# Kernel tuning notes

Hardware: AMD Instinct MI355X
Metric: run time of the kernel (lower is better)

## Reference

```python
import jax, jax.numpy as jnp
import numpy as np

STEPLIM = 20   # module steplim; loop runs while iter <= steplim -> steplim+1 iterations
TOL = 1e-4     # early-stopping tolerance on change in mean NN error


def _nn1(pc1, pc2):
    """1-NN of each point in pc1 [B,N,3] within pc2 [B,M,3] under L2 norm.
    Uses the GEMM form ||a||^2 + ||b||^2 - 2 a.b instead of materializing the
    [B,N,M,3] broadcasted difference tensor. Returns (min_dist [B,N], idx [B,N])."""
    d2 = (jnp.sum(pc1 * pc1, axis=-1)[..., :, None]
          + jnp.sum(pc2 * pc2, axis=-1)[..., None, :]
          - 2.0 * jnp.einsum('bnd,bmd->bnm', pc1, pc2))
    d2 = jnp.maximum(d2, 1e-12)                  # clamp FP cancellation negatives
    idx = jnp.argmin(d2, axis=-1)                # [B, N]
    dmin = jnp.sqrt(jnp.take_along_axis(d2, idx[..., None], axis=-1)[..., 0])
    return dmin, idx


def _kabsch(src, dst):
    """Rigid transform (R, t) minimizing ||R@src + t - dst|| via SVD (EPnP._points_transform)."""
    c1 = jnp.mean(src, axis=-2, keepdims=True)   # [B,1,3]
    c2 = jnp.mean(dst, axis=-2, keepdims=True)
    H = jnp.einsum('bni,bnj->bij', src - c1, dst - c2)          # [B,3,3]
    U, S, Vt = jnp.linalg.svd(H, full_matrices=False)
    det = jnp.linalg.det(jnp.einsum('bki,bjk->bij', Vt, U))     # det(V U^T)
    d = jnp.sign(det)
    D = jnp.stack([jnp.ones_like(d), jnp.ones_like(d), d], axis=-1)  # reflection fix
    R = jnp.einsum('bki,bk,bjk->bij', Vt, D, U)                 # V diag(1,1,d) U^T
    t = c2[..., 0, :] - jnp.einsum('bij,bj->bi', R, c1[..., 0, :])
    return R, t


def _icp(p1, p2):
    B = p1.shape[0]

    def step(carry, _):
        pc, err, done = carry
        dmin, idx = _nn1(pc, p2)
        # errnew = sum(sum(values)/len(values)): mean over batch of per-point sums
        errnew = jnp.sum(dmin) / B
        # source quirk: uses the LAST batch element's indices for all batches
        matched = p2[:, idx[-1], :]                              # [B,N,3]
        R, t = _kabsch(pc, matched)
        pc_new = jnp.einsum('bij,bnj->bni', R, pc) + t[:, None, :]
        # torch loop updates temppc BEFORE the break check, then freezes
        pc_out = jnp.where(done, pc, pc_new)
        err_out = jnp.where(done, err, errnew)
        done_out = done | (jnp.abs(err - errnew) < TOL)
        return (pc_out, err_out, done_out), None

    init = (p1, jnp.asarray(0.0, p1.dtype), jnp.asarray(False))
    (pc, _, _), _ = jax.lax.scan(step, init, None, length=STEPLIM + 1)
    R, t = _kabsch(p1, pc)
    return jnp.concatenate([R, t[..., None]], axis=-1)           # [B,3,4] = [R | t]


def setup_inputs() -> dict:
    key = jax.random.key(0)
    k1, k2 = jax.random.split(key)
    p1 = jax.random.normal(k1, (1, 8192, 3), dtype=jnp.float32)
    p2 = jax.random.normal(k2, (1, 8192, 3), dtype=jnp.float32)
    return {"p1": p1, "p2": p2}


def reference(p1, p2):
    return _icp(p1, p2)
```

## Files before the change

kernel.cpp:

```cpp
#include <hip/hip_runtime.h>
#include <math.h>

#define N_PTS 8192
#define ICP_STEPS 21
#define ICP_TOL 1e-4

#define NBLK 256
#define BSIZE 1024
#define QPW 8

struct IcpCtl {
  double err;
  double Rc[9];
  double tc[3];
  int done;
};

__global__ __launch_bounds__(256) void icp_prep(const float* __restrict__ p2,
                                                float4* __restrict__ p2aug,
                                                IcpCtl* __restrict__ ctl) {
  int t = blockIdx.x * 256 + threadIdx.x;
  float x = p2[3*t], y = p2[3*t+1], z = p2[3*t+2];
  p2aug[t] = make_float4(x, y, z, fmaf(x, x, fmaf(y, y, z*z)));
  if (t == 0) {
    ctl->err = 0.0; ctl->done = 0;
    #pragma unroll
    for (int i = 0; i < 9; ++i) ctl->Rc[i] = (i % 4 == 0) ? 1.0 : 0.0;
    ctl->tc[0] = ctl->tc[1] = ctl->tc[2] = 0.0;
  }
}

__device__ __forceinline__ void kabsch_solve(const double* s, double* R, double* T) {
  const double n = (double)N_PTS;
  const double c1x = s[1]/n, c1y = s[2]/n, c1z = s[3]/n;
  const double c2x = s[4]/n, c2y = s[5]/n, c2z = s[6]/n;
  const double h00 = s[7]  - n*c1x*c2x, h01 = s[8]  - n*c1x*c2y, h02 = s[9]  - n*c1x*c2z;
  const double h10 = s[10] - n*c1y*c2x, h11 = s[11] - n*c1y*c2y, h12 = s[12] - n*c1y*c2z;
  const double h20 = s[13] - n*c1z*c2x, h21 = s[14] - n*c1z*c2y, h22 = s[15] - n*c1z*c2z;

  double a00 = h00*h00 + h10*h10 + h20*h20;
  double a01 = h00*h01 + h10*h11 + h20*h21;
  double a02 = h00*h02 + h10*h12 + h20*h22;
  double a11 = h01*h01 + h11*h11 + h21*h21;
  double a12 = h01*h02 + h11*h12 + h21*h22;
  double a22 = h02*h02 + h12*h12 + h22*h22;

  double v00=1.0, v01=0.0, v02=0.0;
  double v10=0.0, v11=1.0, v12=0.0;
  double v20=0.0, v21=0.0, v22=1.0;

#define ROT3(app, aqq, apq, arp, arq, vpa, vqa, vpb, vqb, vpc, vqc)              \
  {                                                                              \
    double apq_ = apq;                                                           \
    if (fabs(apq_) > 1e-300) {                                                   \
      double tau = (aqq - app) / (2.0 * apq_);                                   \
      double tt  = (tau >= 0.0 ? 1.0 : -1.0) / (fabs(tau) + sqrt(1.0 + tau*tau));\
      double c_  = 1.0 / sqrt(1.0 + tt*tt), sn = tt * c_;                        \
      app -= tt * apq_;  aqq += tt * apq_;  apq = 0.0;                           \
      double t1 = arp, t2 = arq;                                                 \
      arp = c_*t1 - sn*t2;  arq = sn*t1 + c_*t2;                                 \
      t1 = vpa; t2 = vqa; vpa = c_*t1 - sn*t2; vqa = sn*t1 + c_*t2;              \
      t1 = vpb; t2 = vqb; vpb = c_*t1 - sn*t2; vqb = sn*t1 + c_*t2;              \
      t1 = vpc; t2 = vqc; vpc = c_*t1 - sn*t2; vqc = sn*t1 + c_*t2;              \
    }                                                                            \
  }

  #pragma unroll
  for (int sweep = 0; sweep < 6; ++sweep) {
    ROT3(a00, a11, a01, a02, a12, v00, v01, v10, v11, v20, v21);
    ROT3(a00, a22, a02, a01, a12, v00, v02, v10, v12, v20, v22);
    ROT3(a11, a22, a12, a01, a02, v01, v02, v11, v12, v21, v22);
  }
#undef ROT3

  double l0 = a00, l1 = a11, l2 = a22;
  double e0x=v00, e0y=v10, e0z=v20;
  double e1x=v01, e1y=v11, e1z=v21;
  double e2x=v02, e2y=v12, e2z=v22;
#define CSWAP(la, lb, xa, ya, za, xb, yb, zb)                                    \
  if (lb > la) { double t_;                                                      \
    t_ = la; la = lb; lb = t_;  t_ = xa; xa = xb; xb = t_;                       \
    t_ = ya; ya = yb; yb = t_;  t_ = za; za = zb; zb = t_; }
  CSWAP(l0, l1, e0x, e0y, e0z, e1x, e1y, e1z);
  CSWAP(l0, l2, e0x, e0y, e0z, e2x, e2y, e2z);
  CSWAP(l1, l2, e1x, e1y, e1z, e2x, e2y, e2z);
#undef CSWAP

  double detV = e0x*(e1y*e2z - e1z*e2y) - e0y*(e1x*e2z - e1z*e2x)
              + e0z*(e1x*e2y - e1y*e2x);
  const double dsg = (detV >= 0.0) ? 1.0 : -1.0;

  double u0x = h00*e0x + h01*e0y + h02*e0z;
  double u0y = h10*e0x + h11*e0y + h12*e0z;
  double u0z = h20*e0x + h21*e0y + h22*e0z;
  double n0 = sqrt(u0x*u0x + u0y*u0y + u0z*u0z);
  if (!(n0 > 1e-150)) {
    R[0]=1.0; R[1]=0.0; R[2]=0.0; R[3]=0.0; R[4]=1.0; R[5]=0.0;
    R[6]=0.0; R[7]=0.0; R[8]=1.0;
    T[0]=c2x-c1x; T[1]=c2y-c1y; T[2]=c2z-c1z;
    return;
  }
  u0x /= n0; u0y /= n0; u0z /= n0;
  double u1x = h00*e1x + h01*e1y + h02*e1z;
  double u1y = h10*e1x + h11*e1y + h12*e1z;
  double u1z = h20*e1x + h21*e1y + h22*e1z;
  const double d10 = u1x*u0x + u1y*u0y + u1z*u0z;
  u1x -= d10*u0x; u1y -= d10*u0y; u1z -= d10*u0z;
  double n1 = sqrt(u1x*u1x + u1y*u1y + u1z*u1z);
  if (!(n1 > 1e-150)) {
    R[0]=1.0; R[1]=0.0; R[2]=0.0; R[3]=0.0; R[4]=1.0; R[5]=0.0;
    R[6]=0.0; R[7]=0.0; R[8]=1.0;
    T[0]=c2x-c1x; T[1]=c2y-c1y; T[2]=c2z-c1z;
    return;
  }
  u1x /= n1; u1y /= n1; u1z /= n1;
  const double u2x = u0y*u1z - u0z*u1y;
  const double u2y = u0z*u1x - u0x*u1z;
  const double u2z = u0x*u1y - u0y*u1x;

  R[0] = e0x*u0x + e1x*u1x + dsg*e2x*u2x;
  R[1] = e0x*u0y + e1x*u1y + dsg*e2x*u2y;
  R[2] = e0x*u0z + e1x*u1z + dsg*e2x*u2z;
  R[3] = e0y*u0x + e1y*u1x + dsg*e2y*u2x;
  R[4] = e0y*u0y + e1y*u1y + dsg*e2y*u2y;
  R[5] = e0y*u0z + e1y*u1z + dsg*e2y*u2z;
  R[6] = e0z*u0x + e1z*u1x + dsg*e2z*u2x;
  R[7] = e0z*u0y + e1z*u1y + dsg*e2z*u2y;
  R[8] = e0z*u0z + e1z*u1z + dsg*e2z*u2z;
  T[0] = c2x - (R[0]*c1x + R[1]*c1y + R[2]*c1z);
  T[1] = c2y - (R[3]*c1x + R[4]*c1y + R[5]*c1z);
  T[2] = c2z - (R[6]*c1x + R[7]*c1y + R[8]*c1z);
}

__global__ __launch_bounds__(BSIZE, 4) void icp_iter(const float* __restrict__ p1,
                                                     const float4* __restrict__ p2aug,
                                                     const IcpCtl* __restrict__ ctl,
                                                     double* __restrict__ part) {
  if (ctl->done) return;
  __shared__ float4 cand[N_PTS];
  __shared__ unsigned long long pkbuf[32][4];
  __shared__ float4 qlds[32];
  __shared__ double pairbuf[32][17];

  const int tid  = threadIdx.x;
  const int lane = tid & 63;
  const int w    = tid >> 6;
  const int g    = w >> 2;
  const int s    = w & 3;

  #pragma unroll
  for (int k = 0; k < 8; ++k) {
    const int i = (k << 10) + tid;
    cand[i] = p2aug[i];
  }

  const double R0 = ctl->Rc[0], R1 = ctl->Rc[1], R2 = ctl->Rc[2];
  const double R3 = ctl->Rc[3], R4 = ctl->Rc[4], R5 = ctl->Rc[5];
  const double R6 = ctl->Rc[6], R7 = ctl->Rc[7], R8 = ctl->Rc[8];
  const double T0 = ctl->tc[0], T1 = ctl->tc[1], T2 = ctl->tc[2];

  const int qbase = (blockIdx.x << 5) + (g << 3);
  float axv[QPW], ayv[QPW], azv[QPW], best[QPW];
  int bidx[QPW];
  float qxr[QPW], qyr[QPW], qzr[QPW];
  #pragma unroll
  for (int j = 0; j < QPW; ++j) {
    const int q = qbase + j;
    const double X = (double)p1[3*q], Y = (double)p1[3*q+1], Z = (double)p1[3*q+2];
    qxr[j] = (float)(R0*X + R1*Y + R2*Z + T0);
    qyr[j] = (float)(R3*X + R4*Y + R5*Z + T1);
    qzr[j] = (float)(R6*X + R7*Y + R8*Z + T2);
    axv[j] = -2.f*qxr[j]; ayv[j] = -2.f*qyr[j]; azv[j] = -2.f*qzr[j];
    best[j] = __builtin_inff(); bidx[j] = 0;
  }
  if (s == 0 && lane == 0) {
    #pragma unroll
    for (int j = 0; j < QPW; ++j)
      qlds[(g << 3) + j] = make_float4(qxr[j], qyr[j], qzr[j], 0.f);
  }
  __syncthreads();

  const int cb = s << 11;
  #pragma unroll 8
  for (int k = 0; k < 32; ++k) {
    const int cidx = cb + (k << 6) + lane;
    float4 c = cand[cidx];
    #pragma unroll
    for (int j = 0; j < QPW; ++j) {
      float d = fmaf(axv[j], c.x, fmaf(ayv[j], c.y, fmaf(azv[j], c.z, c.w)));
      if (d < best[j]) { best[j] = d; bidx[j] = cidx; }
    }
  }

  unsigned long long pk[QPW];
  #pragma unroll
  for (int j = 0; j < QPW; ++j) {
    unsigned u = __float_as_uint(best[j]);
    u ^= (unsigned)((int)u >> 31) | 0x80000000u;
    pk[j] = ((unsigned long long)u << 32) | (unsigned)bidx[j];
  }
  #pragma unroll
  for (int j = 0; j < QPW; ++j) {
    #pragma unroll
    for (int o = 1; o < 64; o <<= 1) {
      unsigned long long other = __shfl_xor(pk[j], o, 64);
      pk[j] = (other < pk[j]) ? other : pk[j];
    }
  }
  if (lane == 0) {
    #pragma unroll
    for (int j = 0; j < QPW; ++j)
      pkbuf[(g << 3) + j][s] = pk[j];
  }
  __syncthreads();

  if (tid < 32) {
    unsigned long long m = pkbuf[tid][0];
    unsigned long long m1 = pkbuf[tid][1]; m = (m1 < m) ? m1 : m;
    unsigned long long m2 = pkbuf[tid][2]; m = (m2 < m) ? m2 : m;
    unsigned long long m3 = pkbuf[tid][3]; m = (m3 < m) ? m3 : m;
    const unsigned idx = (unsigned)(m & 0xffffffffull);
    const float4 q4 = qlds[tid];
    const float4 b4 = cand[idx];
    const double ax = q4.x, ay = q4.y, az = q4.z;
    const double bx = b4.x, by = b4.y, bz = b4.z;
    const double d2 = (ax*ax + ay*ay + az*az) + (bx*bx + by*by + bz*bz)
                    - 2.0*(ax*bx + ay*by + az*bz);
    pairbuf[tid][0]  = sqrt(fmax(d2, 1e-12));
    pairbuf[tid][1]  = ax;    pairbuf[tid][2]  = ay;    pairbuf[tid][3]  = az;
    pairbuf[tid][4]  = bx;    pairbuf[tid][5]  = by;    pairbuf[tid][6]  = bz;
    pairbuf[tid][7]  = ax*bx; pairbuf[tid][8]  = ax*by; pairbuf[tid][9]  = ax*bz;
    pairbuf[tid][10] = ay*bx; pairbuf[tid][11] = ay*by; pairbuf[tid][12] = ay*bz;
    pairbuf[tid][13] = az*bx; pairbuf[tid][14] = az*by; pairbuf[tid][15] = az*bz;
  }
  __syncthreads();

  if (tid < 16) {
    double ssum = 0.0;
    #pragma unroll
    for (int i = 0; i < 32; ++i) ssum += pairbuf[i][tid];
    part[(blockIdx.x << 4) + tid] = ssum;
  }
}

__device__ __forceinline__ void block_reduce16(double* v, double* tot, double* lds) {
  const int lane = threadIdx.x & 63;
  const int w    = threadIdx.x >> 6;
  #pragma unroll
  for (int q = 0; q < 16; ++q) {
    double x = v[q];
    for (int o = 32; o > 0; o >>= 1) x += __shfl_down(x, o, 64);
    if (lane == 0) lds[w*16 + q] = x;
  }
  __syncthreads();
  if (threadIdx.x < 16)
    tot[threadIdx.x] = lds[threadIdx.x] + lds[16 + threadIdx.x]
                     + lds[32 + threadIdx.x] + lds[48 + threadIdx.x];
  __syncthreads();
}

__global__ __launch_bounds__(256) void icp_solve(IcpCtl* __restrict__ ctl,
                                                 const double* __restrict__ part,
                                                 float* __restrict__ out) {
  if (ctl->done) return;
  __shared__ double lds[64];
  __shared__ double tot[16];
  double v[16];
  const double* row = part + (threadIdx.x << 4);
  #pragma unroll
  for (int c = 0; c < 16; ++c) v[c] = row[c];
  block_reduce16(v, tot, lds);

  if (threadIdx.x == 0) {
    double s[16];
    #pragma unroll
    for (int i = 0; i < 16; ++i) s[i] = tot[i];
    double R[9], T[3];
    kabsch_solve(s, R, T);
    double Rc[9], tc[3], Rn[9], tn[3];
    #pragma unroll
    for (int i = 0; i < 9; ++i) Rc[i] = ctl->Rc[i];
    #pragma unroll
    for (int i = 0; i < 3; ++i) tc[i] = ctl->tc[i];
    #pragma unroll
    for (int i = 0; i < 3; ++i) {
      #pragma unroll
      for (int j = 0; j < 3; ++j)
        Rn[3*i+j] = R[3*i+0]*Rc[0+j] + R[3*i+1]*Rc[3+j] + R[3*i+2]*Rc[6+j];
      tn[i] = R[3*i+0]*tc[0] + R[3*i+1]*tc[1] + R[3*i+2]*tc[2] + T[i];
    }
    #pragma unroll
    for (int i = 0; i < 9; ++i) ctl->Rc[i] = Rn[i];
    #pragma unroll
    for (int i = 0; i < 3; ++i) ctl->tc[i] = tn[i];
    const double errnew = s[0];
    ctl->done = (fabs(ctl->err - errnew) < ICP_TOL) ? 1 : 0;
    ctl->err  = errnew;
    #pragma unroll
    for (int i = 0; i < 3; ++i) {
      out[4*i + 0] = (float)Rn[3*i + 0];
      out[4*i + 1] = (float)Rn[3*i + 1];
      out[4*i + 2] = (float)Rn[3*i + 2];
      out[4*i + 3] = (float)tn[i];
    }
  }
}

extern "C" void kernel_launch(void* const* d_in, const int* in_sizes, int n_in,
                              void* d_out, int out_size, void* d_ws, size_t ws_size,
                              hipStream_t stream) {
  const float* p1 = (const float*)d_in[0];
  const float* p2 = (const float*)d_in[1];
  float* out = (float*)d_out;

  char* ws = (char*)d_ws;
  float4* p2aug = (float4*)ws;
  IcpCtl* ctl   = (IcpCtl*)(ws + 128*1024);
  double* part  = (double*)(ws + 128*1024 + 512);

  icp_prep<<<N_PTS/256, 256, 0, stream>>>(p2, p2aug, ctl);
  for (int it = 0; it < ICP_STEPS; ++it) {
    icp_iter<<<NBLK, BSIZE, 0, stream>>>(p1, p2aug, ctl, part);
    icp_solve<<<1, 256, 0, stream>>>(ctl, part, out);
  }
}
```

Baseline: 552.2 us.

## Fuse per-iteration Kabsch solve into NN kernel via last-block atomic ticket

Drops the separate single-block solve kernel. Each block now atomically adds its 16 partial sums into a global accumulator, and a ticket counter picks the last block to finish, which runs the Kabsch solve, updates the pose and resets the accumulator. This halves the number of kernel launches per ICP step and removes the launch gap and serial reduction kernel between steps. In exchange it adds contention on 16 double atomics and relies on memory-ordering correctness. Summation order is now nondeterministic across runs.

```diff
diff --git a/kernel.cpp b/kernel.cpp
--- a/kernel.cpp
+++ b/kernel.cpp
@@ -8,22 +8,26 @@
 #define NBLK 256
 #define BSIZE 1024
 #define QPW 8
+#define ACC_STRIDE 8
 
 struct IcpCtl {
   double err;
   double Rc[9];
   double tc[3];
   int done;
+  unsigned ticket;
 };
 
 __global__ __launch_bounds__(256) void icp_prep(const float* __restrict__ p2,
                                                 float4* __restrict__ p2aug,
-                                                IcpCtl* __restrict__ ctl) {
+                                                IcpCtl* __restrict__ ctl,
+                                                double* __restrict__ acc) {
   int t = blockIdx.x * 256 + threadIdx.x;
   float x = p2[3*t], y = p2[3*t+1], z = p2[3*t+2];
   p2aug[t] = make_float4(x, y, z, fmaf(x, x, fmaf(y, y, z*z)));
+  if (t < 16 * ACC_STRIDE) acc[t] = 0.0;
   if (t == 0) {
-    ctl->err = 0.0; ctl->done = 0;
+    ctl->err = 0.0; ctl->done = 0; ctl->ticket = 0u;
     #pragma unroll
     for (int i = 0; i < 9; ++i) ctl->Rc[i] = (i % 4 == 0) ? 1.0 : 0.0;
     ctl->tc[0] = ctl->tc[1] = ctl->tc[2] = 0.0;
@@ -134,13 +138,16 @@
 
 __global__ __launch_bounds__(BSIZE, 4) void icp_iter(const float* __restrict__ p1,
                                                      const float4* __restrict__ p2aug,
-                                                     const IcpCtl* __restrict__ ctl,
-                                                     double* __restrict__ part) {
+                                                     IcpCtl* __restrict__ ctl,
+                                                     double* __restrict__ acc,
+                                                     float* __restrict__ out) {
   if (ctl->done) return;
   __shared__ float4 cand[N_PTS];
   __shared__ unsigned long long pkbuf[32][4];
   __shared__ float4 qlds[32];
   __shared__ double pairbuf[32][17];
+  __shared__ double tot[16];
+  __shared__ int lastFlag;
 
   const int tid  = threadIdx.x;
   const int lane = tid & 63;
@@ -239,49 +246,28 @@
     double ssum = 0.0;
     #pragma unroll
     for (int i = 0; i < 32; ++i) ssum += pairbuf[i][tid];
-    part[(blockIdx.x << 4) + tid] = ssum;
-  }
-}
-
-__device__ __forceinline__ void block_reduce16(double* v, double* tot, double* lds) {
-  const int lane = threadIdx.x & 63;
-  const int w    = threadIdx.x >> 6;
-  #pragma unroll
-  for (int q = 0; q < 16; ++q) {
-    double x = v[q];
-    for (int o = 32; o > 0; o >>= 1) x += __shfl_down(x, o, 64);
-    if (lane == 0) lds[w*16 + q] = x;
-  }
-  __syncthreads();
-  if (threadIdx.x < 16)
-    tot[threadIdx.x] = lds[threadIdx.x] + lds[16 + threadIdx.x]
-                     + lds[32 + threadIdx.x] + lds[48 + threadIdx.x];
-  __syncthreads();
-}
-
-__global__ __launch_bounds__(256) void icp_solve(IcpCtl* __restrict__ ctl,
-                                                 const double* __restrict__ part,
-                                                 float* __restrict__ out) {
-  if (ctl->done) return;
-  __shared__ double lds[64];
-  __shared__ double tot[16];
-  double v[16];
-  const double* row = part + (threadIdx.x << 4);
-  #pragma unroll
-  for (int c = 0; c < 16; ++c) v[c] = row[c];
-  block_reduce16(v, tot, lds);
-
-  if (threadIdx.x == 0) {
-    double s[16];
-    #pragma unroll
-    for (int i = 0; i < 16; ++i) s[i] = tot[i];
+    atomicAdd(acc + tid * ACC_STRIDE, ssum);
+  }
+  if (tid == 0) {
+    asm volatile("s_waitcnt vmcnt(0)" ::: "memory");
+    unsigned old = __hip_atomic_fetch_add(&ctl->ticket, 1u,
+                      __ATOMIC_RELAXED, __HIP_MEMORY_SCOPE_AGENT);
+    lastFlag = (old == NBLK - 1u) ? 1 : 0;
+  }
+  __syncthreads();
+  if (!lastFlag) return;
+
+  if (tid < 16) tot[tid] = atomicAdd(acc + tid * ACC_STRIDE, 0.0);
+  __syncthreads();
+  if (tid == 0) {
+    double sm[16];
+    #pragma unroll
+    for (int i = 0; i < 16; ++i) sm[i] = tot[i];
     double R[9], T[3];
-    kabsch_solve(s, R, T);
-    double Rc[9], tc[3], Rn[9], tn[3];
-    #pragma unroll
-    for (int i = 0; i < 9; ++i) Rc[i] = ctl->Rc[i];
-    #pragma unroll
-    for (int i = 0; i < 3; ++i) tc[i] = ctl->tc[i];
+    kabsch_solve(sm, R, T);
+    double Rc[9] = {R0,R1,R2,R3,R4,R5,R6,R7,R8};
+    double tc[3] = {T0,T1,T2};
+    double Rn[9], tn[3];
     #pragma unroll
     for (int i = 0; i < 3; ++i) {
       #pragma unroll
@@ -293,7 +279,7 @@
     for (int i = 0; i < 9; ++i) ctl->Rc[i] = Rn[i];
     #pragma unroll
     for (int i = 0; i < 3; ++i) ctl->tc[i] = tn[i];
-    const double errnew = s[0];
+    const double errnew = sm[0];
     ctl->done = (fabs(ctl->err - errnew) < ICP_TOL) ? 1 : 0;
     ctl->err  = errnew;
     #pragma unroll
@@ -303,6 +289,9 @@
       out[4*i + 2] = (float)Rn[3*i + 2];
       out[4*i + 3] = (float)tn[i];
     }
+    #pragma unroll
+    for (int i = 0; i < 16; ++i) acc[i * ACC_STRIDE] = 0.0;
+    ctl->ticket = 0u;
   }
 }
 
@@ -316,11 +305,9 @@
   char* ws = (char*)d_ws;
   float4* p2aug = (float4*)ws;
   IcpCtl* ctl   = (IcpCtl*)(ws + 128*1024);
-  double* part  = (double*)(ws + 128*1024 + 512);
-
-  icp_prep<<<N_PTS/256, 256, 0, stream>>>(p2, p2aug, ctl);
-  for (int it = 0; it < ICP_STEPS; ++it) {
-    icp_iter<<<NBLK, BSIZE, 0, stream>>>(p1, p2aug, ctl, part);
-    icp_solve<<<1, 256, 0, stream>>>(ctl, part, out);
-  }
+  double* acc   = (double*)(ws + 128*1024 + 512);
+
+  icp_prep<<<N_PTS/256, 256, 0, stream>>>(p2, p2aug, ctl, acc);
+  for (int it = 0; it < ICP_STEPS; ++it)
+    icp_iter<<<NBLK, BSIZE, 0, stream>>>(p1, p2aug, ctl, acc, out);
 }
```

Measured after the change: 585.4 us. 1.06x slower.

## Fuse per-iteration Kabsch solve into the next NN-search kernel with ping-pong state

Applied to the files above, without the earlier changes.

Removes the separate single-block solve launch after each ICP iteration. Every block of the next iteration kernel now reduces the previous iteration's partial sums, solves the Kabsch transform and composes it redundantly, then proceeds with its nearest-neighbour search. State and partial buffers are double-buffered so reads and writes don't race, and a final small kernel produces the output. This trades about 20 launch and serialization gaps for redundant per-block reduction work and extra L2 reads of the partials. The occupancy hint in launch_bounds is also dropped.

```diff
diff --git a/kernel.cpp b/kernel.cpp
--- a/kernel.cpp
+++ b/kernel.cpp
@@ -9,24 +9,24 @@
 #define BSIZE 1024
 #define QPW 8
 
-struct IcpCtl {
-  double err;
+struct IcpSt {
   double Rc[9];
   double tc[3];
+  double err;
   int done;
 };
 
 __global__ __launch_bounds__(256) void icp_prep(const float* __restrict__ p2,
                                                 float4* __restrict__ p2aug,
-                                                IcpCtl* __restrict__ ctl) {
+                                                IcpSt* __restrict__ st0) {
   int t = blockIdx.x * 256 + threadIdx.x;
   float x = p2[3*t], y = p2[3*t+1], z = p2[3*t+2];
   p2aug[t] = make_float4(x, y, z, fmaf(x, x, fmaf(y, y, z*z)));
   if (t == 0) {
-    ctl->err = 0.0; ctl->done = 0;
-    #pragma unroll
-    for (int i = 0; i < 9; ++i) ctl->Rc[i] = (i % 4 == 0) ? 1.0 : 0.0;
-    ctl->tc[0] = ctl->tc[1] = ctl->tc[2] = 0.0;
+    #pragma unroll
+    for (int i = 0; i < 9; ++i) st0->Rc[i] = (i % 4 == 0) ? 1.0 : 0.0;
+    st0->tc[0] = st0->tc[1] = st0->tc[2] = 0.0;
+    st0->err = 0.0; st0->done = 0;
   }
 }
 
@@ -132,12 +132,38 @@
   T[2] = c2z - (R[6]*c1x + R[7]*c1y + R[8]*c1z);
 }
 
-__global__ __launch_bounds__(BSIZE, 4) void icp_iter(const float* __restrict__ p1,
-                                                     const float4* __restrict__ p2aug,
-                                                     const IcpCtl* __restrict__ ctl,
-                                                     double* __restrict__ part) {
-  if (ctl->done) return;
+__device__ __forceinline__ void solve_compose(const double* s, const IcpSt* stIn,
+                                              double* Rn, double* tn,
+                                              double* errnew, int* dn) {
+  double R[9], T[3];
+  kabsch_solve(s, R, T);
+  double Rc[9], tc[3];
+  #pragma unroll
+  for (int i = 0; i < 9; ++i) Rc[i] = stIn->Rc[i];
+  #pragma unroll
+  for (int i = 0; i < 3; ++i) tc[i] = stIn->tc[i];
+  #pragma unroll
+  for (int i = 0; i < 3; ++i) {
+    #pragma unroll
+    for (int j = 0; j < 3; ++j)
+      Rn[3*i+j] = R[3*i+0]*Rc[0+j] + R[3*i+1]*Rc[3+j] + R[3*i+2]*Rc[6+j];
+    tn[i] = R[3*i+0]*tc[0] + R[3*i+1]*tc[1] + R[3*i+2]*tc[2] + T[i];
+  }
+  *errnew = s[0];
+  *dn = (fabs(stIn->err - *errnew) < ICP_TOL) ? 1 : 0;
+}
+
+__global__ __launch_bounds__(BSIZE) void icp_iter(const float* __restrict__ p1,
+                                                  const float4* __restrict__ p2aug,
+                                                  const IcpSt* __restrict__ stIn,
+                                                  IcpSt* __restrict__ stOut,
+                                                  const double* __restrict__ partIn,
+                                                  double* __restrict__ partOut,
+                                                  const int k) {
   __shared__ float4 cand[N_PTS];
+  __shared__ double redbuf[64];
+  __shared__ double RT[12];
+  __shared__ int sdone;
   __shared__ unsigned long long pkbuf[32][4];
   __shared__ float4 qlds[32];
   __shared__ double pairbuf[32][17];
@@ -148,16 +174,72 @@
   const int g    = w >> 2;
   const int s    = w & 3;
 
-  #pragma unroll
-  for (int k = 0; k < 8; ++k) {
-    const int i = (k << 10) + tid;
+  if (stIn->done) {
+    if (blockIdx.x == 0 && tid == 0) {
+      #pragma unroll
+      for (int i = 0; i < 9; ++i) stOut->Rc[i] = stIn->Rc[i];
+      #pragma unroll
+      for (int i = 0; i < 3; ++i) stOut->tc[i] = stIn->tc[i];
+      stOut->err = stIn->err; stOut->done = 1;
+    }
+    return;
+  }
+
+  #pragma unroll
+  for (int k2 = 0; k2 < 8; ++k2) {
+    const int i = (k2 << 10) + tid;
     cand[i] = p2aug[i];
   }
 
-  const double R0 = ctl->Rc[0], R1 = ctl->Rc[1], R2 = ctl->Rc[2];
-  const double R3 = ctl->Rc[3], R4 = ctl->Rc[4], R5 = ctl->Rc[5];
-  const double R6 = ctl->Rc[6], R7 = ctl->Rc[7], R8 = ctl->Rc[8];
-  const double T0 = ctl->tc[0], T1 = ctl->tc[1], T2 = ctl->tc[2];
+  double R0, R1, R2, R3, R4, R5, R6, R7, R8, T0, T1, T2;
+  if (k > 0) {
+    double vv[16];
+    if (tid < 256) {
+      const double* row = partIn + (tid << 4);
+      #pragma unroll
+      for (int c = 0; c < 16; ++c) vv[c] = row[c];
+    } else {
+      #pragma unroll
+      for (int c = 0; c < 16; ++c) vv[c] = 0.0;
+    }
+    if (w < 4) {
+      #pragma unroll
+      for (int q = 0; q < 16; ++q) {
+        double x = vv[q];
+        for (int o = 32; o > 0; o >>= 1) x += __shfl_down(x, o, 64);
+        if (lane == 0) redbuf[w*16 + q] = x;
+      }
+    }
+    __syncthreads();
+    if (tid == 0) {
+      double sm[16];
+      #pragma unroll
+      for (int i = 0; i < 16; ++i)
+        sm[i] = redbuf[i] + redbuf[16+i] + redbuf[32+i] + redbuf[48+i];
+      double Rn[9], tn[3], errnew; int dn;
+      solve_compose(sm, stIn, Rn, tn, &errnew, &dn);
+      #pragma unroll
+      for (int i = 0; i < 9; ++i) stOut->Rc[i] = Rn[i];
+      #pragma unroll
+      for (int i = 0; i < 3; ++i) stOut->tc[i] = tn[i];
+      stOut->err = errnew; stOut->done = dn;
+      #pragma unroll
+      for (int i = 0; i < 9; ++i) RT[i] = Rn[i];
+      RT[9] = tn[0]; RT[10] = tn[1]; RT[11] = tn[2];
+      sdone = dn;
+    }
+    __syncthreads();
+    if (sdone) return;
+    R0 = RT[0]; R1 = RT[1]; R2 = RT[2];
+    R3 = RT[3]; R4 = RT[4]; R5 = RT[5];
+    R6 = RT[6]; R7 = RT[7]; R8 = RT[8];
+    T0 = RT[9]; T1 = RT[10]; T2 = RT[11];
+  } else {
+    R0 = stIn->Rc[0]; R1 = stIn->Rc[1]; R2 = stIn->Rc[2];
+    R3 = stIn->Rc[3]; R4 = stIn->Rc[4]; R5 = stIn->Rc[5];
+    R6 = stIn->Rc[6]; R7 = stIn->Rc[7]; R8 = stIn->Rc[8];
+    T0 = stIn->tc[0]; T1 = stIn->tc[1]; T2 = stIn->tc[2];
+  }
 
   const int qbase = (blockIdx.x << 5) + (g << 3);
   float axv[QPW], ayv[QPW], azv[QPW], best[QPW];
@@ -182,8 +264,8 @@
 
   const int cb = s << 11;
   #pragma unroll 8
-  for (int k = 0; k < 32; ++k) {
-    const int cidx = cb + (k << 6) + lane;
+  for (int kk = 0; kk < 32; ++kk) {
+    const int cidx = cb + (kk << 6) + lane;
     float4 c = cand[cidx];
     #pragma unroll
     for (int j = 0; j < QPW; ++j) {
@@ -239,13 +321,35 @@
     double ssum = 0.0;
     #pragma unroll
     for (int i = 0; i < 32; ++i) ssum += pairbuf[i][tid];
-    part[(blockIdx.x << 4) + tid] = ssum;
-  }
-}
-
-__device__ __forceinline__ void block_reduce16(double* v, double* tot, double* lds) {
+    partOut[(blockIdx.x << 4) + tid] = ssum;
+  }
+}
+
+__global__ __launch_bounds__(256) void icp_final(const IcpSt* __restrict__ stIn,
+                                                 const double* __restrict__ partIn,
+                                                 float* __restrict__ out) {
+  __shared__ double lds[64];
+  __shared__ double tot[16];
   const int lane = threadIdx.x & 63;
   const int w    = threadIdx.x >> 6;
+
+  if (stIn->done) {
+    if (threadIdx.x == 0) {
+      #pragma unroll
+      for (int i = 0; i < 3; ++i) {
+        out[4*i + 0] = (float)stIn->Rc[3*i + 0];
+        out[4*i + 1] = (float)stIn->Rc[3*i + 1];
+        out[4*i + 2] = (float)stIn->Rc[3*i + 2];
+        out[4*i + 3] = (float)stIn->tc[i];
+      }
+    }
+    return;
+  }
+
+  double v[16];
+  const double* row = partIn + (threadIdx.x << 4);
+  #pragma unroll
+  for (int c = 0; c < 16; ++c) v[c] = row[c];
   #pragma unroll
   for (int q = 0; q < 16; ++q) {
     double x = v[q];
@@ -257,45 +361,13 @@
     tot[threadIdx.x] = lds[threadIdx.x] + lds[16 + threadIdx.x]
                      + lds[32 + threadIdx.x] + lds[48 + threadIdx.x];
   __syncthreads();
-}
-
-__global__ __launch_bounds__(256) void icp_solve(IcpCtl* __restrict__ ctl,
-                                                 const double* __restrict__ part,
-                                                 float* __restrict__ out) {
-  if (ctl->done) return;
-  __shared__ double lds[64];
-  __shared__ double tot[16];
-  double v[16];
-  const double* row = part + (threadIdx.x << 4);
-  #pragma unroll
-  for (int c = 0; c < 16; ++c) v[c] = row[c];
-  block_reduce16(v, tot, lds);
 
   if (threadIdx.x == 0) {
-    double s[16];
-    #pragma unroll
-    for (int i = 0; i < 16; ++i) s[i] = tot[i];
-    double R[9], T[3];
-    kabsch_solve(s, R, T);
-    double Rc[9], tc[3], Rn[9], tn[3];
-    #pragma unroll
-    for (int i = 0; i < 9; ++i) Rc[i] = ctl->Rc[i];
-    #pragma unroll
-    for (int i = 0; i < 3; ++i) tc[i] = ctl->tc[i];
-    #pragma unroll
-    for (int i = 0; i < 3; ++i) {
-      #pragma unroll
-      for (int j = 0; j < 3; ++j)
-        Rn[3*i+j] = R[3*i+0]*Rc[0+j] + R[3*i+1]*Rc[3+j] + R[3*i+2]*Rc[6+j];
-      tn[i] = R[3*i+0]*tc[0] + R[3*i+1]*tc[1] + R[3*i+2]*tc[2] + T[i];
-    }
-    #pragma unroll
-    for (int i = 0; i < 9; ++i) ctl->Rc[i] = Rn[i];
-    #pragma unroll
-    for (int i = 0; i < 3; ++i) ctl->tc[i] = tn[i];
-    const double errnew = s[0];
-    ctl->done = (fabs(ctl->err - errnew) < ICP_TOL) ? 1 : 0;
-    ctl->err  = errnew;
+    double sm[16];
+    #pragma unroll
+    for (int i = 0; i < 16; ++i) sm[i] = tot[i];
+    double Rn[9], tn[3], errnew; int dn;
+    solve_compose(sm, stIn, Rn, tn, &errnew, &dn);
     #pragma unroll
     for (int i = 0; i < 3; ++i) {
       out[4*i + 0] = (float)Rn[3*i + 0];
@@ -315,12 +387,22 @@
 
   char* ws = (char*)d_ws;
   float4* p2aug = (float4*)ws;
-  IcpCtl* ctl   = (IcpCtl*)(ws + 128*1024);
-  double* part  = (double*)(ws + 128*1024 + 512);
-
-  icp_prep<<<N_PTS/256, 256, 0, stream>>>(p2, p2aug, ctl);
-  for (int it = 0; it < ICP_STEPS; ++it) {
-    icp_iter<<<NBLK, BSIZE, 0, stream>>>(p1, p2aug, ctl, part);
-    icp_solve<<<1, 256, 0, stream>>>(ctl, part, out);
-  }
-}
+  IcpSt* st0    = (IcpSt*)(ws + 128*1024);
+  IcpSt* st1    = (IcpSt*)(ws + 128*1024 + 256);
+  double* part0 = (double*)(ws + 128*1024 + 1024);
+  double* part1 = (double*)(ws + 128*1024 + 1024 + 32*1024);
+
+  IcpSt* st[2]    = { st0, st1 };
+  double* part[2] = { part0, part1 };
+
+  icp_prep<<<N_PTS/256, 256, 0, stream>>>(p2, p2aug, st0);
+  for (int k = 0; k < ICP_STEPS; ++k) {
+    const IcpSt* stIn   = (k == 0) ? st0 : st[(k-1) & 1];
+    IcpSt* stOut        = st[k & 1];
+    const double* pIn   = part[(k+1) & 1];
+    double* pOut        = part[k & 1];
+    if (k == 0) stOut = st1;
+    icp_iter<<<NBLK, BSIZE, 0, stream>>>(p1, p2aug, stIn, stOut, pIn, pOut, k);
+  }
+  icp_final<<<1, 256, 0, stream>>>(st[0], part[0], out);
+}
```

Result: no change. 546.7 us (-1.0%).

## Replace full-LDS NN kernel with chunked, register-prefetched 256-thread blocks

Applied to the files above, without the earlier changes.

The nearest-neighbour kernel changes from 256 blocks of 1024 threads, each staging all 8192 candidates in LDS, to 512 blocks of 256 threads. Each block handles 16 queries, four per wave, and streams candidates through a 2048-entry LDS chunk, prefetching the next chunk into registers while the current one is scanned. The aim is to cut the per-block LDS footprint and the cost of the big up-front load, giving more resident blocks and overlapping global loads with compute. In exchange each wave now scans all candidates for only 4 queries, so candidate reuse per LDS read drops. The solve kernel is widened to 512 threads to reduce the doubled number of partials.

```diff
diff --git a/kernel.cpp b/kernel.cpp
--- a/kernel.cpp
+++ b/kernel.cpp
@@ -5,9 +5,11 @@
 #define ICP_STEPS 21
 #define ICP_TOL 1e-4
 
-#define NBLK 256
-#define BSIZE 1024
-#define QPW 8
+#define NNB 512
+#define QPB 16
+#define QPWv 4
+#define CH 2048
+#define NCH 4
 
 struct IcpCtl {
   double err;
@@ -27,6 +29,113 @@
     #pragma unroll
     for (int i = 0; i < 9; ++i) ctl->Rc[i] = (i % 4 == 0) ? 1.0 : 0.0;
     ctl->tc[0] = ctl->tc[1] = ctl->tc[2] = 0.0;
+  }
+}
+
+__global__ __launch_bounds__(256) void icp_nn(const float* __restrict__ p1,
+                                              const float4* __restrict__ p2aug,
+                                              const IcpCtl* __restrict__ ctl,
+                                              double* __restrict__ part) {
+  if (ctl->done) return;
+  __shared__ float4 cand[CH];
+  __shared__ unsigned long long pkbuf[4][5];
+  __shared__ float4 qlds[QPB];
+  __shared__ double pairbuf[QPB][17];
+
+  const int tid  = threadIdx.x;
+  const int lane = tid & 63;
+  const int w    = tid >> 6;
+
+  const double R0 = ctl->Rc[0], R1 = ctl->Rc[1], R2 = ctl->Rc[2];
+  const double R3 = ctl->Rc[3], R4 = ctl->Rc[4], R5 = ctl->Rc[5];
+  const double R6 = ctl->Rc[6], R7 = ctl->Rc[7], R8 = ctl->Rc[8];
+  const double T0 = ctl->tc[0], T1 = ctl->tc[1], T2 = ctl->tc[2];
+
+  const int qb = blockIdx.x * QPB + (w << 2);
+  float axv[QPWv], ayv[QPWv], azv[QPWv], best[QPWv];
+  int bidx[QPWv];
+  #pragma unroll
+  for (int j = 0; j < QPWv; ++j) {
+    const int q = qb + j;
+    const double X = (double)p1[3*q], Y = (double)p1[3*q+1], Z = (double)p1[3*q+2];
+    const float qx = (float)(R0*X + R1*Y + R2*Z + T0);
+    const float qy = (float)(R3*X + R4*Y + R5*Z + T1);
+    const float qz = (float)(R6*X + R7*Y + R8*Z + T2);
+    axv[j] = -2.f*qx; ayv[j] = -2.f*qy; azv[j] = -2.f*qz;
+    best[j] = __builtin_inff(); bidx[j] = 0;
+    if (lane == 0) qlds[(w << 2) + j] = make_float4(qx, qy, qz, 0.f);
+  }
+
+  float4 pf[8];
+  #pragma unroll
+  for (int k = 0; k < 8; ++k) pf[k] = p2aug[(k << 8) + tid];
+  for (int cb = 0; cb < NCH; ++cb) {
+    #pragma unroll
+    for (int k = 0; k < 8; ++k) cand[(k << 8) + tid] = pf[k];
+    __syncthreads();
+    if (cb + 1 < NCH) {
+      #pragma unroll
+      for (int k = 0; k < 8; ++k)
+        pf[k] = p2aug[((cb + 1) << 11) + (k << 8) + tid];
+    }
+    const int cbase = cb << 11;
+    #pragma unroll 8
+    for (int kk = 0; kk < 32; ++kk) {
+      const int cidx = cbase + (kk << 6) + lane;
+      float4 c = cand[(kk << 6) + lane];
+      #pragma unroll
+      for (int j = 0; j < QPWv; ++j) {
+        float d = fmaf(axv[j], c.x, fmaf(ayv[j], c.y, fmaf(azv[j], c.z, c.w)));
+        if (d < best[j]) { best[j] = d; bidx[j] = cidx; }
+      }
+    }
+    __syncthreads();
+  }
+
+  unsigned long long pk[QPWv];
+  #pragma unroll
+  for (int j = 0; j < QPWv; ++j) {
+    unsigned u = __float_as_uint(best[j]);
+    u ^= (unsigned)((int)u >> 31) | 0x80000000u;
+    pk[j] = ((unsigned long long)u << 32) | (unsigned)bidx[j];
+  }
+  #pragma unroll
+  for (int j = 0; j < QPWv; ++j) {
+    #pragma unroll
+    for (int o = 1; o < 64; o <<= 1) {
+      unsigned long long other = __shfl_xor(pk[j], o, 64);
+      pk[j] = (other < pk[j]) ? other : pk[j];
+    }
+  }
+  if (lane == 0) {
+    #pragma unroll
+    for (int j = 0; j < QPWv; ++j) pkbuf[w][j] = pk[j];
+  }
+  __syncthreads();
+
+  if (tid < QPB) {
+    const unsigned long long m = pkbuf[tid >> 2][tid & 3];
+    const unsigned idx = (unsigned)(m & 0xffffffffull);
+    const float4 q4 = qlds[tid];
+    const float4 b4 = p2aug[idx];
+    const double ax = q4.x, ay = q4.y, az = q4.z;
+    const double bx = b4.x, by = b4.y, bz = b4.z;
+    const double d2 = (ax*ax + ay*ay + az*az) + (bx*bx + by*by + bz*bz)
+                    - 2.0*(ax*bx + ay*by + az*bz);
+    pairbuf[tid][0]  = sqrt(fmax(d2, 1e-12));
+    pairbuf[tid][1]  = ax;    pairbuf[tid][2]  = ay;    pairbuf[tid][3]  = az;
+    pairbuf[tid][4]  = bx;    pairbuf[tid][5]  = by;    pairbuf[tid][6]  = bz;
+    pairbuf[tid][7]  = ax*bx; pairbuf[tid][8]  = ax*by; pairbuf[tid][9]  = ax*bz;
+    pairbuf[tid][10] = ay*bx; pairbuf[tid][11] = ay*by; pairbuf[tid][12] = ay*bz;
+    pairbuf[tid][13] = az*bx; pairbuf[tid][14] = az*by; pairbuf[tid][15] = az*bz;
+  }
+  __syncthreads();
+
+  if (tid < 16) {
+    double s = 0.0;
+    #pragma unroll
+    for (int i = 0; i < QPB; ++i) s += pairbuf[i][tid];
+    part[(blockIdx.x << 4) + tid] = s;
   }
 }
 
@@ -132,120 +241,20 @@
   T[2] = c2z - (R[6]*c1x + R[7]*c1y + R[8]*c1z);
 }
 
-__global__ __launch_bounds__(BSIZE, 4) void icp_iter(const float* __restrict__ p1,
-                                                     const float4* __restrict__ p2aug,
-                                                     const IcpCtl* __restrict__ ctl,
-                                                     double* __restrict__ part) {
+__global__ __launch_bounds__(512) void icp_solve(IcpCtl* __restrict__ ctl,
+                                                 const double* __restrict__ part,
+                                                 float* __restrict__ out) {
   if (ctl->done) return;
-  __shared__ float4 cand[N_PTS];
-  __shared__ unsigned long long pkbuf[32][4];
-  __shared__ float4 qlds[32];
-  __shared__ double pairbuf[32][17];
-
+  __shared__ double lds[8 * 16];
+  __shared__ double tot[16];
   const int tid  = threadIdx.x;
   const int lane = tid & 63;
   const int w    = tid >> 6;
-  const int g    = w >> 2;
-  const int s    = w & 3;
-
-  #pragma unroll
-  for (int k = 0; k < 8; ++k) {
-    const int i = (k << 10) + tid;
-    cand[i] = p2aug[i];
-  }
-
-  const double R0 = ctl->Rc[0], R1 = ctl->Rc[1], R2 = ctl->Rc[2];
-  const double R3 = ctl->Rc[3], R4 = ctl->Rc[4], R5 = ctl->Rc[5];
-  const double R6 = ctl->Rc[6], R7 = ctl->Rc[7], R8 = ctl->Rc[8];
-  const double T0 = ctl->tc[0], T1 = ctl->tc[1], T2 = ctl->tc[2];
-
-  const int qbase = (blockIdx.x << 5) + (g << 3);
-  float axv[QPW], ayv[QPW], azv[QPW], best[QPW];
-  int bidx[QPW];
-  float qxr[QPW], qyr[QPW], qzr[QPW];
-  #pragma unroll
-  for (int j = 0; j < QPW; ++j) {
-    const int q = qbase + j;
-    const double X = (double)p1[3*q], Y = (double)p1[3*q+1], Z = (double)p1[3*q+2];
-    qxr[j] = (float)(R0*X + R1*Y + R2*Z + T0);
-    qyr[j] = (float)(R3*X + R4*Y + R5*Z + T1);
-    qzr[j] = (float)(R6*X + R7*Y + R8*Z + T2);
-    axv[j] = -2.f*qxr[j]; ayv[j] = -2.f*qyr[j]; azv[j] = -2.f*qzr[j];
-    best[j] = __builtin_inff(); bidx[j] = 0;
-  }
-  if (s == 0 && lane == 0) {
-    #pragma unroll
-    for (int j = 0; j < QPW; ++j)
-      qlds[(g << 3) + j] = make_float4(qxr[j], qyr[j], qzr[j], 0.f);
-  }
-  __syncthreads();
-
-  const int cb = s << 11;
-  #pragma unroll 8
-  for (int k = 0; k < 32; ++k) {
-    const int cidx = cb + (k << 6) + lane;
-    float4 c = cand[cidx];
-    #pragma unroll
-    for (int j = 0; j < QPW; ++j) {
-      float d = fmaf(axv[j], c.x, fmaf(ayv[j], c.y, fmaf(azv[j], c.z, c.w)));
-      if (d < best[j]) { best[j] = d; bidx[j] = cidx; }
-    }
-  }
-
-  unsigned long long pk[QPW];
-  #pragma unroll
-  for (int j = 0; j < QPW; ++j) {
-    unsigned u = __float_as_uint(best[j]);
-    u ^= (unsigned)((int)u >> 31) | 0x80000000u;
-    pk[j] = ((unsigned long long)u << 32) | (unsigned)bidx[j];
-  }
-  #pragma unroll
-  for (int j = 0; j < QPW; ++j) {
-    #pragma unroll
-    for (int o = 1; o < 64; o <<= 1) {
-      unsigned long long other = __shfl_xor(pk[j], o, 64);
-      pk[j] = (other < pk[j]) ? other : pk[j];
-    }
-  }
-  if (lane == 0) {
-    #pragma unroll
-    for (int j = 0; j < QPW; ++j)
-      pkbuf[(g << 3) + j][s] = pk[j];
-  }
-  __syncthreads();
-
-  if (tid < 32) {
-    unsigned long long m = pkbuf[tid][0];
-    unsigned long long m1 = pkbuf[tid][1]; m = (m1 < m) ? m1 : m;
-    unsigned long long m2 = pkbuf[tid][2]; m = (m2 < m) ? m2 : m;
-    unsigned long long m3 = pkbuf[tid][3]; m = (m3 < m) ? m3 : m;
-    const unsigned idx = (unsigned)(m & 0xffffffffull);
-    const float4 q4 = qlds[tid];
-    const float4 b4 = cand[idx];
-    const double ax = q4.x, ay = q4.y, az = q4.z;
-    const double bx = b4.x, by = b4.y, bz = b4.z;
-    const double d2 = (ax*ax + ay*ay + az*az) + (bx*bx + by*by + bz*bz)
-                    - 2.0*(ax*bx + ay*by + az*bz);
-    pairbuf[tid][0]  = sqrt(fmax(d2, 1e-12));
-    pairbuf[tid][1]  = ax;    pairbuf[tid][2]  = ay;    pairbuf[tid][3]  = az;
-    pairbuf[tid][4]  = bx;    pairbuf[tid][5]  = by;    pairbuf[tid][6]  = bz;
-    pairbuf[tid][7]  = ax*bx; pairbuf[tid][8]  = ax*by; pairbuf[tid][9]  = ax*bz;
-    pairbuf[tid][10] = ay*bx; pairbuf[tid][11] = ay*by; pairbuf[tid][12] = ay*bz;
-    pairbuf[tid][13] = az*bx; pairbuf[tid][14] = az*by; pairbuf[tid][15] = az*bz;
-  }
-  __syncthreads();
-
-  if (tid < 16) {
-    double ssum = 0.0;
-    #pragma unroll
-    for (int i = 0; i < 32; ++i) ssum += pairbuf[i][tid];
-    part[(blockIdx.x << 4) + tid] = ssum;
-  }
-}
-
-__device__ __forceinline__ void block_reduce16(double* v, double* tot, double* lds) {
-  const int lane = threadIdx.x & 63;
-  const int w    = threadIdx.x >> 6;
+
+  double v[16];
+  const double* row = part + (tid << 4);
+  #pragma unroll
+  for (int c = 0; c < 16; ++c) v[c] = row[c];
   #pragma unroll
   for (int q = 0; q < 16; ++q) {
     double x = v[q];
@@ -253,30 +262,20 @@
     if (lane == 0) lds[w*16 + q] = x;
   }
   __syncthreads();
-  if (threadIdx.x < 16)
-    tot[threadIdx.x] = lds[threadIdx.x] + lds[16 + threadIdx.x]
-                     + lds[32 + threadIdx.x] + lds[48 + threadIdx.x];
+  if (tid < 16) {
+    double s = 0.0;
+    #pragma unroll
+    for (int r = 0; r < 8; ++r) s += lds[r*16 + tid];
+    tot[tid] = s;
+  }
   __syncthreads();
-}
-
-__global__ __launch_bounds__(256) void icp_solve(IcpCtl* __restrict__ ctl,
-                                                 const double* __restrict__ part,
-                                                 float* __restrict__ out) {
-  if (ctl->done) return;
-  __shared__ double lds[64];
-  __shared__ double tot[16];
-  double v[16];
-  const double* row = part + (threadIdx.x << 4);
-  #pragma unroll
-  for (int c = 0; c < 16; ++c) v[c] = row[c];
-  block_reduce16(v, tot, lds);
-
-  if (threadIdx.x == 0) {
-    double s[16];
-    #pragma unroll
-    for (int i = 0; i < 16; ++i) s[i] = tot[i];
+
+  if (tid == 0) {
+    double sm[16];
+    #pragma unroll
+    for (int i = 0; i < 16; ++i) sm[i] = tot[i];
     double R[9], T[3];
-    kabsch_solve(s, R, T);
+    kabsch_solve(sm, R, T);
     double Rc[9], tc[3], Rn[9], tn[3];
     #pragma unroll
     for (int i = 0; i < 9; ++i) Rc[i] = ctl->Rc[i];
@@ -293,7 +292,7 @@
     for (int i = 0; i < 9; ++i) ctl->Rc[i] = Rn[i];
     #pragma unroll
     for (int i = 0; i < 3; ++i) ctl->tc[i] = tn[i];
-    const double errnew = s[0];
+    const double errnew = sm[0];
     ctl->done = (fabs(ctl->err - errnew) < ICP_TOL) ? 1 : 0;
     ctl->err  = errnew;
     #pragma unroll
@@ -316,11 +315,11 @@
   char* ws = (char*)d_ws;
   float4* p2aug = (float4*)ws;
   IcpCtl* ctl   = (IcpCtl*)(ws + 128*1024);
-  double* part  = (double*)(ws + 128*1024 + 512);
+  double* part  = (double*)(ws + 132*1024);
 
   icp_prep<<<N_PTS/256, 256, 0, stream>>>(p2, p2aug, ctl);
   for (int it = 0; it < ICP_STEPS; ++it) {
-    icp_iter<<<NBLK, BSIZE, 0, stream>>>(p1, p2aug, ctl, part);
-    icp_solve<<<1, 256, 0, stream>>>(ctl, part, out);
-  }
-}
+    icp_nn<<<NNB, 256, 0, stream>>>(p1, p2aug, ctl, part);
+    icp_solve<<<1, 512, 0, stream>>>(ctl, part, out);
+  }
+}
```

Result: slower. 815.5 us (+47.7%).
